# Kernel optimization log

Hardware: AMD Instinct MI355X
Metric: run time of the kernel (lower is better)

The kernel has to match this reference:

```python
import jax, jax.numpy as jnp
import numpy as np

N_NODES = 50000


def sage_conv(x, src, dst, Wl, bl, Wr):
    # PyG SAGEConv (aggr='mean'): out_i = Wl @ mean_{j in N(i)} x_j + bl + Wr @ x_i
    msg = x[src]                                              # [E, d] gather
    agg = jax.ops.segment_sum(msg, dst, num_segments=N_NODES)  # [N, d]
    cnt = jax.ops.segment_sum(jnp.ones((src.shape[0],), x.dtype), dst,
                              num_segments=N_NODES)
    mean = agg / jnp.maximum(cnt, 1.0)[:, None]
    return mean @ Wl.T + bl + x @ Wr.T


def graph_forward(x, edge_index, W1l, b1, W1r, W2l, b2, W2r):
    src, dst = edge_index[0], edge_index[1]
    h = jnp.tanh(sage_conv(x, src, dst, W1l, b1, W1r))
    return jnp.tanh(sage_conv(h, src, dst, W2l, b2, W2r))


def setup_inputs() -> dict:
    key = jax.random.key(0)
    ks = jax.random.split(key, 16)
    E = 800000
    IN, HID, OUT = 128, 256, 128
    s = lambda fan: 1.0 / np.sqrt(fan)
    inp = {
        'x0': jax.random.normal(ks[0], (N_NODES, IN), jnp.float32),
        'x1': jax.random.normal(ks[1], (N_NODES, IN), jnp.float32),
        'edge_index0': jax.random.randint(ks[2], (2, E), 0, N_NODES),
        'edge_index1': jax.random.randint(ks[3], (2, E), 0, N_NODES),
    }
    for g, base in ((0, 4), (1, 10)):
        inp[f'W1l_{g}'] = jax.random.normal(ks[base + 0], (HID, IN), jnp.float32) * s(IN)
        inp[f'b1_{g}'] = jnp.zeros((HID,), jnp.float32)
        inp[f'W1r_{g}'] = jax.random.normal(ks[base + 1], (HID, IN), jnp.float32) * s(IN)
        inp[f'W2l_{g}'] = jax.random.normal(ks[base + 2], (OUT, HID), jnp.float32) * s(HID)
        inp[f'b2_{g}'] = jnp.zeros((OUT,), jnp.float32)
        inp[f'W2r_{g}'] = jax.random.normal(ks[base + 3], (OUT, HID), jnp.float32) * s(HID)
    return inp


def reference(x0, x1, edge_index0, edge_index1,
              W1l_0, b1_0, W1r_0, W2l_0, b2_0, W2r_0,
              W1l_1, b1_1, W1r_1, W2l_1, b2_1, W2r_1):
    out0 = graph_forward(x0, edge_index0, W1l_0, b1_0, W1r_0, W2l_0, b2_0, W2r_0)
    out1 = graph_forward(x1, edge_index1, W1l_1, b1_1, W1r_1, W2l_1, b2_1, W2r_1)
    return jnp.concatenate([out0, out1], axis=0)
```

## Files before the change

kernel.cpp:

```cpp
#include <hip/hip_runtime.h>
#include <cstddef>

#define N_NODES 50000
#define N_EDGES 800000
#define CAP 64
#define XU (N_NODES * 16)
#define XRNG ((N_NODES + 7) / 8)

typedef __attribute__((ext_vector_type(8))) _Float16 half8;
typedef __attribute__((ext_vector_type(2))) _Float16 half2v;
typedef __attribute__((ext_vector_type(4))) float f32x4;
typedef __attribute__((ext_vector_type(4))) float f4v;

__device__ __forceinline__ float fast_tanh(float x) {
    float t = __expf(2.0f * x);
    return 1.0f - 2.0f / (t + 1.0f);
}

__global__ __launch_bounds__(256) void prep_k(
        const int* __restrict__ src0, const int* __restrict__ dst0,
        const int* __restrict__ src1, const int* __restrict__ dst1,
        int* __restrict__ cnt, int* __restrict__ adj,
        const float* __restrict__ x0, const float* __restrict__ x1,
        const float* __restrict__ w00, const float* __restrict__ w01,
        const float* __restrict__ w02, const float* __restrict__ w03,
        const float* __restrict__ w10, const float* __restrict__ w11,
        const float* __restrict__ w12, const float* __restrict__ w13,
        _Float16* __restrict__ xd, _Float16* __restrict__ wd) {
    const int triple = blockIdx.x >> 3;
    const int role3 = triple % 3;
    const int slot = (triple / 3) * 8 + (blockIdx.x & 7);
    if (role3 < 2) {
        const int fs = role3 * 4096 + slot;
        const int g = fs >> 12;
        const int b = fs & 4095;
        const int* src = g ? src1 : src0;
        const int* dst = g ? dst1 : dst0;
        int* cg = cnt + g * N_NODES;
        int* ag = adj + (size_t)g * N_NODES * CAP;
        const int grp = b & 7;
        const int lo = grp * XRNG, hi = lo + XRNG;
        for (int e = (b >> 3) * 256 + threadIdx.x; e < N_EDGES; e += 131072) {
            int d = __builtin_nontemporal_load(dst + e);
            if (d >= lo && d < hi) {
                int sv = __builtin_nontemporal_load(src + e);
                int c = atomicAdd(&cg[d], 1);
                if (c < CAP) ag[d * CAP + c] = sv;
            }
        }
    } else {
        const int total = 2 * XU + 32768;
        for (int i = slot * 256 + threadIdx.x; i < total; i += 4096 * 256) {
            const float* s; _Float16* d;
            if (i < 2 * XU) {
                int g = i >= XU ? 1 : 0;
                int l = i - g * XU;
                s = (g ? x1 : x0) + (size_t)l * 8;
                d = xd + (size_t)g * ((size_t)N_NODES * 256) + (size_t)l * 8;
            } else {
                int w = i - 2 * XU;
                int g = w >> 14, m = (w >> 12) & 3, l = w & 4095;
                const float* wm;
                if (g == 0) wm = (m == 0) ? w00 : (m == 1) ? w01 : (m == 2) ? w02 : w03;
                else        wm = (m == 0) ? w10 : (m == 1) ? w11 : (m == 2) ? w12 : w13;
                s = wm + (size_t)l * 8;
                d = wd + (size_t)g * 131072 + (size_t)m * 32768 + (size_t)l * 8;
            }
            f4v v0 = __builtin_nontemporal_load((const f4v*)s);
            f4v v1 = __builtin_nontemporal_load((const f4v*)s + 1);
            half8 o;
            o[0] = (_Float16)v0[0]; o[1] = (_Float16)v0[1];
            o[2] = (_Float16)v0[2]; o[3] = (_Float16)v0[3];
            o[4] = (_Float16)v1[0]; o[5] = (_Float16)v1[1];
            o[6] = (_Float16)v1[2]; o[7] = (_Float16)v1[3];
            *(half8*)d = o;
        }
    }
}

template <int OUTM, int RSU>
__global__ __launch_bounds__(256) void gather_mean_k(
        const unsigned* __restrict__ Xu, size_t xgs,
        const int* __restrict__ cnt, const int* __restrict__ adj,
        unsigned* __restrict__ outm, size_t ogs,
        const float* __restrict__ bias0, const float* __restrict__ bias1,
        float* __restrict__ outf, int N) {
    const int g = blockIdx.y;
    int gw = blockIdx.x * 4 + (threadIdx.x >> 6);
    if (gw >= N) return;
    const int lane = threadIdx.x & 63;
    const int deg0 = cnt[g * N_NODES + gw];
    const int deg = deg0 < CAP ? deg0 : CAP;
    const int* aj = adj + (size_t)g * N_NODES * CAP + (size_t)gw * CAP;
    const unsigned* Xl = Xu + (size_t)g * xgs + lane;
    float sx = 0.f, sy = 0.f;
    int n = 0;
    for (; n + 16 <= deg; n += 16) {
        unsigned u0  = Xl[(size_t)aj[n     ] * RSU];
        unsigned u1  = Xl[(size_t)aj[n +  1] * RSU];
        unsigned u2  = Xl[(size_t)aj[n +  2] * RSU];
        unsigned u3  = Xl[(size_t)aj[n +  3] * RSU];
        unsigned u4  = Xl[(size_t)aj[n +  4] * RSU];
        unsigned u5  = Xl[(size_t)aj[n +  5] * RSU];
        unsigned u6  = Xl[(size_t)aj[n +  6] * RSU];
        unsigned u7  = Xl[(size_t)aj[n +  7] * RSU];
        unsigned u8  = Xl[(size_t)aj[n +  8] * RSU];
        unsigned u9  = Xl[(size_t)aj[n +  9] * RSU];
        unsigned u10 = Xl[(size_t)aj[n + 10] * RSU];
        unsigned u11 = Xl[(size_t)aj[n + 11] * RSU];
        unsigned u12 = Xl[(size_t)aj[n + 12] * RSU];
        unsigned u13 = Xl[(size_t)aj[n + 13] * RSU];
        unsigned u14 = Xl[(size_t)aj[n + 14] * RSU];
        unsigned u15 = Xl[(size_t)aj[n + 15] * RSU];
        half2v h0  = __builtin_bit_cast(half2v, u0);
        half2v h1  = __builtin_bit_cast(half2v, u1);
        half2v h2  = __builtin_bit_cast(half2v, u2);
        half2v h3  = __builtin_bit_cast(half2v, u3);
        half2v h4  = __builtin_bit_cast(half2v, u4);
        half2v h5  = __builtin_bit_cast(half2v, u5);
        half2v h6  = __builtin_bit_cast(half2v, u6);
        half2v h7  = __builtin_bit_cast(half2v, u7);
        half2v h8  = __builtin_bit_cast(half2v, u8);
        half2v h9  = __builtin_bit_cast(half2v, u9);
        half2v h10 = __builtin_bit_cast(half2v, u10);
        half2v h11 = __builtin_bit_cast(half2v, u11);
        half2v h12 = __builtin_bit_cast(half2v, u12);
        half2v h13 = __builtin_bit_cast(half2v, u13);
        half2v h14 = __builtin_bit_cast(half2v, u14);
        half2v h15 = __builtin_bit_cast(half2v, u15);
        sx += (float)h0.x + (float)h1.x + (float)h2.x + (float)h3.x
            + (float)h4.x + (float)h5.x + (float)h6.x + (float)h7.x
            + (float)h8.x + (float)h9.x + (float)h10.x + (float)h11.x
            + (float)h12.x + (float)h13.x + (float)h14.x + (float)h15.x;
        sy += (float)h0.y + (float)h1.y + (float)h2.y + (float)h3.y
            + (float)h4.y + (float)h5.y + (float)h6.y + (float)h7.y
            + (float)h8.y + (float)h9.y + (float)h10.y + (float)h11.y
            + (float)h12.y + (float)h13.y + (float)h14.y + (float)h15.y;
    }
    for (; n + 4 <= deg; n += 4) {
        unsigned u0 = Xl[(size_t)aj[n    ] * RSU];
        unsigned u1 = Xl[(size_t)aj[n + 1] * RSU];
        unsigned u2 = Xl[(size_t)aj[n + 2] * RSU];
        unsigned u3 = Xl[(size_t)aj[n + 3] * RSU];
        half2v h0 = __builtin_bit_cast(half2v, u0);
        half2v h1 = __builtin_bit_cast(half2v, u1);
        half2v h2 = __builtin_bit_cast(half2v, u2);
        half2v h3 = __builtin_bit_cast(half2v, u3);
        sx += (float)h0.x + (float)h1.x + (float)h2.x + (float)h3.x;
        sy += (float)h0.y + (float)h1.y + (float)h2.y + (float)h3.y;
    }
    for (; n < deg; n++) {
        unsigned u = Xl[(size_t)aj[n] * RSU];
        half2v h = __builtin_bit_cast(half2v, u);
        sx += (float)h.x;
        sy += (float)h.y;
    }
    float inv = 1.0f / (float)(deg0 > 0 ? deg0 : 1);
    float mx = sx * inv, my = sy * inv;
    if (OUTM == 0) {
        half2v o;
        o.x = (_Float16)mx; o.y = (_Float16)my;
        outm[(size_t)g * ogs + (size_t)gw * 64 + lane] =
            __builtin_bit_cast(unsigned, o);
    } else {
        unsigned pu = Xu[(size_t)g * xgs + (size_t)gw * 128 + 64 + lane];
        half2v ph = __builtin_bit_cast(half2v, pu);
        const float* bias = g ? bias1 : bias0;
        float2 bb = ((const float2*)bias)[lane];
        float2 o;
        o.x = fast_tanh(mx + (float)ph.x + bb.x);
        o.y = fast_tanh(my + (float)ph.y + bb.y);
        ((float2*)(outf + (size_t)g * N_NODES * 128))[(size_t)gw * 64 + lane] = o;
    }
}

#define TM 128
#define TN 64
#define TK 32
#define LSTR 40
#define OSTR 72
#define SMEM_BYTES (TM * OSTR * 2)

template <bool TANH>
__global__ __launch_bounds__(256)
void gemm_f16_k(const _Float16* __restrict__ A1a, const _Float16* __restrict__ A1b,
                const _Float16* __restrict__ B1a, const _Float16* __restrict__ B1b,
                int K1,
                const _Float16* __restrict__ A2a, const _Float16* __restrict__ A2b,
                const _Float16* __restrict__ B2a, const _Float16* __restrict__ B2b,
                int K2,
                const float* __restrict__ biasa, const float* __restrict__ biasb,
                _Float16* __restrict__ outa, _Float16* __restrict__ outb,
                int N, int Md) {
    const int gz = blockIdx.z;
    const _Float16* A1 = gz ? A1b : A1a;
    const _Float16* B1 = gz ? B1b : B1a;
    const _Float16* A2 = gz ? A2b : A2a;
    const _Float16* B2 = gz ? B2b : B2a;
    const float* bias  = gz ? biasb : biasa;
    _Float16* outh     = gz ? outb : outa;

    __shared__ char smem[SMEM_BYTES];
    _Float16 (*sA)[LSTR] = reinterpret_cast<_Float16(*)[LSTR]>(smem);
    _Float16 (*sB)[LSTR] = reinterpret_cast<_Float16(*)[LSTR]>(smem + TM * LSTR * 2);
    _Float16 (*sO)[OSTR] = reinterpret_cast<_Float16(*)[OSTR]>(smem);

    const int tid = threadIdx.x;
    const int lane = tid & 63;
    const int wave = tid >> 6;
    const int waveM = (wave & 1) * 64;
    const int waveN = (wave >> 1) * 32;
    const int rowBase = blockIdx.y * TM;
    const int colBase = blockIdx.x * TN;
    const int Ktot = K1 + K2;

    const int r0 = tid >> 2, c0 = tid & 3;
    const int r1 = r0 + 64;
    const int gr0 = rowBase + r0, gr1 = rowBase + r1;

    f32x4 acc[4][2] = {};
    half8 pA0, pA1, pB0;

    auto load_tile = [&](int k0) {
        const _Float16 *A, *B; int ko, ld;
        if (k0 < K1) { A = A1; B = B1; ko = k0;      ld = K1; }
        else         { A = A2; B = B2; ko = k0 - K1; ld = K2; }
        half8 z = {(_Float16)0, (_Float16)0, (_Float16)0, (_Float16)0,
                   (_Float16)0, (_Float16)0, (_Float16)0, (_Float16)0};
        size_t a0 = (size_t)gr0 * ld + ko + c0 * 8;
        size_t a1 = (size_t)gr1 * ld + ko + c0 * 8;
        pA0 = gr0 < N ? *(const half8*)(A + a0) : z;
        pA1 = gr1 < N ? *(const half8*)(A + a1) : z;
        pB0 = *(const half8*)(B + (size_t)(colBase + r0) * ld + ko + c0 * 8);
    };
    auto store_tile = [&]() {
        *(half8*)&sA[r0][c0 * 8] = pA0;
        *(half8*)&sA[r1][c0 * 8] = pA1;
        *(half8*)&sB[r0][c0 * 8] = pB0;
    };

    const int fm = lane & 15;
    const int fq = (lane >> 4) * 8;
    half8 fa[4], fb[2];
    auto read_frags = [&]() {
        #pragma unroll
        for (int mi = 0; mi < 4; mi++)
            fa[mi] = *(const half8*)&sA[waveM + mi * 16 + fm][fq];
        #pragma unroll
        for (int ni = 0; ni < 2; ni++)
            fb[ni] = *(const half8*)&sB[waveN + ni * 16 + fm][fq];
    };
    auto mfma_all = [&]() {
        #pragma unroll
        for (int mi = 0; mi < 4; mi++)
            #pragma unroll
            for (int ni = 0; ni < 2; ni++)
                acc[mi][ni] = __builtin_amdgcn_mfma_f32_16x16x32_f16(
                    fa[mi], fb[ni], acc[mi][ni], 0, 0, 0);
    };

    load_tile(0);
    store_tile();
    __syncthreads();

    for (int k0 = TK; k0 < Ktot; k0 += TK) {
        read_frags();
        load_tile(k0);
        mfma_all();
        __syncthreads();
        store_tile();
        __syncthreads();
    }
    read_frags();
    mfma_all();

    __syncthreads();
    {
        const int lr0 = waveM + (lane >> 4) * 4;
        const int lc0 = waveN + fm;
        #pragma unroll
        for (int ni = 0; ni < 2; ni++) {
            float bv = bias ? bias[colBase + lc0 + ni * 16] : 0.0f;
            #pragma unroll
            for (int mi = 0; mi < 4; mi++)
                #pragma unroll
                for (int r = 0; r < 4; r++) {
                    float v = acc[mi][ni][r] + bv;
                    if (TANH) v = fast_tanh(v);
                    sO[lr0 + mi * 16 + r][lc0 + ni * 16] = (_Float16)v;
                }
        }
    }
    __syncthreads();
    {
        const int rr = tid >> 3;
        const int cc = (tid & 7) * 8;
        #pragma unroll
        for (int p = 0; p < 4; p++) {
            int row = p * 32 + rr;
            int grow = rowBase + row;
            if (grow < N)
                *(half8*)(outh + (size_t)grow * Md + colBase + cc) =
                    *(const half8*)&sO[row][cc];
        }
    }
}

extern "C" void kernel_launch(void* const* d_in, const int* in_sizes, int n_in,
                              void* d_out, int out_size, void* d_ws, size_t ws_size,
                              hipStream_t stream) {
    const int N = N_NODES, E = N_EDGES;

    const float* x[2]   = {(const float*)d_in[0],  (const float*)d_in[1]};
    const int*   ei[2]  = {(const int*)d_in[2],    (const int*)d_in[3]};
    const float* W1l[2] = {(const float*)d_in[4],  (const float*)d_in[10]};
    const float* b1[2]  = {(const float*)d_in[5],  (const float*)d_in[11]};
    const float* W1r[2] = {(const float*)d_in[6],  (const float*)d_in[12]};
    const float* W2l[2] = {(const float*)d_in[7],  (const float*)d_in[13]};
    const float* b2[2]  = {(const float*)d_in[8],  (const float*)d_in[14]};
    const float* W2r[2] = {(const float*)d_in[9],  (const float*)d_in[15]};
    float* out = (float*)d_out;

    char* wsb = (char*)d_ws;
    const size_t MiB = 1u << 20;
    int*      cnt  = (int*)(wsb);
    int*      adj  = (int*)(wsb + 1 * MiB);
    _Float16* Wh   = (_Float16*)(wsb + 27 * MiB);
    _Float16* feat = (_Float16*)(wsb + 28 * MiB);
    _Float16* h16  = (_Float16*)(wsb + 80 * MiB);

    const size_t FGS  = (size_t)N * 256;
    const size_t WGS  = 131072;
    const size_t HSTR = (size_t)N * 256;

    const int gemm_rows = (N + TM - 1) / TM;
    const int agg_x = N / 4;

    (void)hipMemsetAsync(cnt, 0, 2 * (size_t)N * sizeof(int), stream);
    prep_k<<<12288, 256, 0, stream>>>(
        ei[0], ei[0] + E, ei[1], ei[1] + E, cnt, adj,
        x[0], x[1],
        W1l[0], W1r[0], W2l[0], W2r[0],
        W1l[1], W1r[1], W2l[1], W2r[1],
        feat, Wh);

    gather_mean_k<0, 64><<<dim3(agg_x, 2), 256, 0, stream>>>(
        (const unsigned*)feat, FGS / 2, cnt, adj,
        (unsigned*)(feat + (size_t)N * 128), FGS / 2,
        nullptr, nullptr, nullptr, N);

    _Float16* x16g[2]   = {feat, feat + FGS};
    _Float16* mean16[2] = {feat + (size_t)N * 128, feat + FGS + (size_t)N * 128};
    _Float16* hz16[2]   = {feat, feat + FGS};
    _Float16* W1l16[2]  = {Wh, Wh + WGS};
    _Float16* W1r16[2]  = {Wh + 32768, Wh + WGS + 32768};
    _Float16* W2cat[2]  = {Wh + 65536, Wh + WGS + 65536};

    if (ws_size >= (size_t)132 * MiB) {
        _Float16* h0 = h16;
        _Float16* h1 = h16 + HSTR;
        gemm_f16_k<true><<<dim3(4, gemm_rows, 2), 256, 0, stream>>>(
            mean16[0], mean16[1], W1l16[0], W1l16[1], 128,
            x16g[0], x16g[1], W1r16[0], W1r16[1], 128,
            b1[0], b1[1], h0, h1, N, 256);
        gemm_f16_k<false><<<dim3(4, gemm_rows, 2), 256, 0, stream>>>(
            h0, h1, W2cat[0], W2cat[1], 256,
            nullptr, nullptr, nullptr, nullptr, 0,
            nullptr, nullptr, hz16[0], hz16[1], N, 256);
    } else {
        for (int g = 0; g < 2; g++) {
            gemm_f16_k<true><<<dim3(4, gemm_rows, 1), 256, 0, stream>>>(
                mean16[g], mean16[g], W1l16[g], W1l16[g], 128,
                x16g[g], x16g[g], W1r16[g], W1r16[g], 128,
                b1[g], b1[g], h16, h16, N, 256);
            gemm_f16_k<false><<<dim3(4, gemm_rows, 1), 256, 0, stream>>>(
                h16, h16, W2cat[g], W2cat[g], 256,
                nullptr, nullptr, nullptr, nullptr, 0,
                nullptr, nullptr, hz16[g], hz16[g], N, 256);
        }
    }

    gather_mean_k<1, 128><<<dim3(agg_x, 2), 256, 0, stream>>>(
        (const unsigned*)feat, FGS / 2, cnt, adj,
        nullptr, 0, b2[0], b2[1], out, N);
}
```

Before: 411.7 us.

## Split second GEMM output into compact z and root planes; regroup adjacency build

The second-layer GEMM now writes its output in two 128-wide planes: the neighbour-projected part z and the root part. This gives the final gather a 256-byte row stride (RSU 64) instead of 512, so each neighbour row fetch covers a denser region and needs fewer cache lines. The root term is read from its own plane. The adjacency-building blocks are also remapped so each block filters a wider destination range (a quarter of the nodes per graph) with a larger edge stride, which halves the redundant scanning of edge lists.

```diff
diff --git a/kernel.cpp b/kernel.cpp
--- a/kernel.cpp
+++ b/kernel.cpp
@@ -29,18 +29,16 @@
         _Float16* __restrict__ xd, _Float16* __restrict__ wd) {
     const int triple = blockIdx.x >> 3;
     const int role3 = triple % 3;
-    const int slot = (triple / 3) * 8 + (blockIdx.x & 7);
+    const int grp = blockIdx.x & 7;
     if (role3 < 2) {
-        const int fs = role3 * 4096 + slot;
-        const int g = fs >> 12;
-        const int b = fs & 4095;
+        const int ftriple = (triple / 3) * 2 + role3;
+        const int g = grp >> 2;
+        const int lo = (grp & 3) * (2 * XRNG), hi = lo + 2 * XRNG;
         const int* src = g ? src1 : src0;
         const int* dst = g ? dst1 : dst0;
         int* cg = cnt + g * N_NODES;
         int* ag = adj + (size_t)g * N_NODES * CAP;
-        const int grp = b & 7;
-        const int lo = grp * XRNG, hi = lo + XRNG;
-        for (int e = (b >> 3) * 256 + threadIdx.x; e < N_EDGES; e += 131072) {
+        for (int e = ftriple * 256 + threadIdx.x; e < N_EDGES; e += 262144) {
             int d = __builtin_nontemporal_load(dst + e);
             if (d >= lo && d < hi) {
                 int sv = __builtin_nontemporal_load(src + e);
@@ -49,6 +47,7 @@
             }
         }
     } else {
+        const int slot = (triple / 3) * 8 + grp;
         const int total = 2 * XU + 32768;
         for (int i = slot * 256 + threadIdx.x; i < total; i += 4096 * 256) {
             const float* s; _Float16* d;
@@ -83,6 +82,7 @@
         const unsigned* __restrict__ Xu, size_t xgs,
         const int* __restrict__ cnt, const int* __restrict__ adj,
         unsigned* __restrict__ outm, size_t ogs,
+        const unsigned* __restrict__ Pu, size_t pgs,
         const float* __restrict__ bias0, const float* __restrict__ bias1,
         float* __restrict__ outf, int N) {
     const int g = blockIdx.y;
@@ -163,7 +163,7 @@
         outm[(size_t)g * ogs + (size_t)gw * 64 + lane] =
             __builtin_bit_cast(unsigned, o);
     } else {
-        unsigned pu = Xu[(size_t)g * xgs + (size_t)gw * 128 + 64 + lane];
+        unsigned pu = Pu[(size_t)g * pgs + (size_t)gw * 64 + lane];
         half2v ph = __builtin_bit_cast(half2v, pu);
         const float* bias = g ? bias1 : bias0;
         float2 bb = ((const float2*)bias)[lane];
@@ -190,15 +190,17 @@
                 const _Float16* __restrict__ B2a, const _Float16* __restrict__ B2b,
                 int K2,
                 const float* __restrict__ biasa, const float* __restrict__ biasb,
-                _Float16* __restrict__ outa, _Float16* __restrict__ outb,
-                int N, int Md) {
+                _Float16* __restrict__ outLoA, _Float16* __restrict__ outLoB,
+                _Float16* __restrict__ outHiA, _Float16* __restrict__ outHiB,
+                int MdLo, int MdHi, int N) {
     const int gz = blockIdx.z;
     const _Float16* A1 = gz ? A1b : A1a;
     const _Float16* B1 = gz ? B1b : B1a;
     const _Float16* A2 = gz ? A2b : A2a;
     const _Float16* B2 = gz ? B2b : B2a;
     const float* bias  = gz ? biasb : biasa;
-    _Float16* outh     = gz ? outb : outa;
+    _Float16* outLo    = gz ? outLoB : outLoA;
+    _Float16* outHi    = gz ? outHiB : outHiA;
 
     __shared__ char smem[SMEM_BYTES];
     _Float16 (*sA)[LSTR] = reinterpret_cast<_Float16(*)[LSTR]>(smem);
@@ -293,6 +295,9 @@
     }
     __syncthreads();
     {
+        _Float16* outp; int Md, cb;
+        if (colBase < 128) { outp = outLo; Md = MdLo; cb = colBase; }
+        else               { outp = outHi; Md = MdHi; cb = colBase - 128; }
         const int rr = tid >> 3;
         const int cc = (tid & 7) * 8;
         #pragma unroll
@@ -300,7 +305,7 @@
             int row = p * 32 + rr;
             int grow = rowBase + row;
             if (grow < N)
-                *(half8*)(outh + (size_t)grow * Md + colBase + cc) =
+                *(half8*)(outp + (size_t)grow * Md + cb + cc) =
                     *(const half8*)&sO[row][cc];
         }
     }
@@ -347,11 +352,12 @@
     gather_mean_k<0, 64><<<dim3(agg_x, 2), 256, 0, stream>>>(
         (const unsigned*)feat, FGS / 2, cnt, adj,
         (unsigned*)(feat + (size_t)N * 128), FGS / 2,
-        nullptr, nullptr, nullptr, N);
+        nullptr, 0, nullptr, nullptr, nullptr, N);
 
     _Float16* x16g[2]   = {feat, feat + FGS};
     _Float16* mean16[2] = {feat + (size_t)N * 128, feat + FGS + (size_t)N * 128};
-    _Float16* hz16[2]   = {feat, feat + FGS};
+    _Float16* z16[2]    = {feat, feat + FGS};
+    _Float16* po16[2]   = {feat + (size_t)N * 128, feat + FGS + (size_t)N * 128};
     _Float16* W1l16[2]  = {Wh, Wh + WGS};
     _Float16* W1r16[2]  = {Wh + 32768, Wh + WGS + 32768};
     _Float16* W2cat[2]  = {Wh + 65536, Wh + WGS + 65536};
@@ -362,25 +368,27 @@
         gemm_f16_k<true><<<dim3(4, gemm_rows, 2), 256, 0, stream>>>(
             mean16[0], mean16[1], W1l16[0], W1l16[1], 128,
             x16g[0], x16g[1], W1r16[0], W1r16[1], 128,
-            b1[0], b1[1], h0, h1, N, 256);
+            b1[0], b1[1], h0, h1, h0 + 128, h1 + 128, 256, 256, N);
         gemm_f16_k<false><<<dim3(4, gemm_rows, 2), 256, 0, stream>>>(
             h0, h1, W2cat[0], W2cat[1], 256,
             nullptr, nullptr, nullptr, nullptr, 0,
-            nullptr, nullptr, hz16[0], hz16[1], N, 256);
+            nullptr, nullptr, z16[0], z16[1], po16[0], po16[1], 128, 128, N);
     } else {
         for (int g = 0; g < 2; g++) {
             gemm_f16_k<true><<<dim3(4, gemm_rows, 1), 256, 0, stream>>>(
                 mean16[g], mean16[g], W1l16[g], W1l16[g], 128,
                 x16g[g], x16g[g], W1r16[g], W1r16[g], 128,
-                b1[g], b1[g], h16, h16, N, 256);
+                b1[g], b1[g], h16, h16, h16 + 128, h16 + 128, 256, 256, N);
             gemm_f16_k<false><<<dim3(4, gemm_rows, 1), 256, 0, stream>>>(
                 h16, h16, W2cat[g], W2cat[g], 256,
                 nullptr, nullptr, nullptr, nullptr, 0,
-                nullptr, nullptr, hz16[g], hz16[g], N, 256);
-        }
-    }
-
-    gather_mean_k<1, 128><<<dim3(agg_x, 2), 256, 0, stream>>>(
+                nullptr, nullptr, z16[g], z16[g], po16[g], po16[g], 128, 128, N);
+        }
+    }
+
+    gather_mean_k<1, 64><<<dim3(agg_x, 2), 256, 0, stream>>>(
         (const unsigned*)feat, FGS / 2, cnt, adj,
-        nullptr, 0, b2[0], b2[1], out, N);
-}
+        nullptr, 0,
+        (const unsigned*)(feat + (size_t)N * 128), FGS / 2,
+        b2[0], b2[1], out, N);
+}
```

Result: faster. 395.7 us (-3.9%).
